# Optimization experiments

Hardware: AMD Instinct MI355X
Metric: run time of the kernel (lower is better)

The kernel has to match this reference:

```python
import jax, jax.numpy as jnp
import numpy as np
import math

EPS = 1e-5

def sinusoidal_pe(seq_len, d_model, dtype=jnp.float32):
    pos = jnp.arange(seq_len, dtype=jnp.float32)[:, None]
    div = jnp.exp(jnp.arange(0, d_model, 2, dtype=jnp.float32) * (-math.log(10000.0) / d_model))
    pe = jnp.zeros((seq_len, d_model), dtype=jnp.float32)
    pe = pe.at[:, 0::2].set(jnp.sin(pos * div))
    pe = pe.at[:, 1::2].set(jnp.cos(pos * div))
    return pe.astype(dtype)

def rel_shift(pos_score):
    # pos_score: [B, H, S, S] -> Transformer-XL relative shift
    B, H, S1, S2 = pos_score.shape
    padded = jnp.pad(pos_score, ((0, 0), (0, 0), (0, 0), (1, 0)))  # [B,H,S1,S2+1]
    return padded.reshape(B, H, S2 + 1, S1)[:, :, 1:, :].reshape(B, H, S1, S2)

def setup_inputs() -> dict:
    key = jax.random.key(0)
    B, S, D, H = 4, 2048, 512, 8
    dh = D // H
    ks = jax.random.split(key, 12)
    scale = 0.02
    inp = {
        'inputs': jax.random.normal(ks[0], (B, S, D), dtype=jnp.float32),
        'gamma': jnp.ones((D,), jnp.float32),
        'beta': jnp.zeros((D,), jnp.float32),
        'Wq': jax.random.normal(ks[1], (D, D), jnp.float32) * scale,
        'bq': jnp.zeros((D,), jnp.float32),
        'Wk': jax.random.normal(ks[2], (D, D), jnp.float32) * scale,
        'bk': jnp.zeros((D,), jnp.float32),
        'Wv': jax.random.normal(ks[3], (D, D), jnp.float32) * scale,
        'bv': jnp.zeros((D,), jnp.float32),
        'Wpos': jax.random.normal(ks[4], (D, D), jnp.float32) * scale,
        'u_bias': jax.random.normal(ks[5], (H, dh), jnp.float32) * scale,
        'v_bias': jax.random.normal(ks[6], (H, dh), jnp.float32) * scale,
        'Wo': jax.random.normal(ks[7], (D, D), jnp.float32) * scale,
        'bo': jnp.zeros((D,), jnp.float32),
    }
    return inp

def reference(inputs, gamma, beta, Wq, bq, Wk, bk, Wv, bv, Wpos, u_bias, v_bias, Wo, bo):
    B, S, D = inputs.shape
    H, dh = u_bias.shape
    # relative positional encoding (same for each batch element)
    pos_emb = sinusoidal_pe(S, D)  # [S, D]
    # pre-norm
    mu = jnp.mean(inputs, axis=-1, keepdims=True)
    var = jnp.var(inputs, axis=-1, keepdims=True)
    x = (inputs - mu) * jax.lax.rsqrt(var + EPS) * gamma + beta
    # projections (torch Linear: y = x @ W.T + b)
    q = (x @ Wq.T + bq).reshape(B, S, H, dh)
    k = (x @ Wk.T + bk).reshape(B, S, H, dh)
    v = (x @ Wv.T + bv).reshape(B, S, H, dh)
    pos = (pos_emb @ Wpos.T).reshape(S, H, dh)
    # content and position scores
    content = jnp.einsum('bshd,bthd->bhst', q + u_bias, k)
    pos_score = jnp.einsum('bshd,thd->bhst', q + v_bias, pos)
    pos_score = rel_shift(pos_score)
    score = (content + pos_score) / jnp.sqrt(jnp.float32(D))
    attn = jax.nn.softmax(score, axis=-1)  # dropout = identity (eval mode)
    ctx = jnp.einsum('bhst,bthd->bshd', attn, v).reshape(B, S, D)
    out = ctx @ Wo.T + bo
    return out  # module dropout = identity in eval
```

## Files before the change

### kernel.cpp

```cpp
#include <hip/hip_runtime.h>
#include <math.h>

typedef unsigned short u16;
typedef unsigned int u32;
typedef __bf16 bf16x8 __attribute__((ext_vector_type(8)));
typedef float f32x4 __attribute__((ext_vector_type(4)));

#define SEQ 2048
#define DM  512
#define NH  8
#define DH  64
#define SP  2064
#define PE_ROWS 2304
#define MFMA(a,b,c) __builtin_amdgcn_mfma_f32_16x16x32_bf16(a,b,c,0,0,0)

__device__ __forceinline__ u16 f2bf(float f) {
  union { float f; u32 u; } x; x.f = f;
  u32 u = x.u;
  u32 r = u + 0x7fffu + ((u >> 16) & 1u);
  return (u16)(r >> 16);
}
__device__ __forceinline__ float bf2f(u16 h) {
  union { u32 u; float f; } x; x.u = ((u32)h) << 16;
  return x.f;
}
__device__ __forceinline__ f32x4 fzero() { f32x4 z = {0.f,0.f,0.f,0.f}; return z; }

__device__ __forceinline__ void gl16(const u16* g, u16* l) {
  __builtin_amdgcn_global_load_lds((const __attribute__((address_space(1))) void*)g,
                                   (__attribute__((address_space(3))) void*)l, 16, 0, 0);
}

__global__ __launch_bounds__(256) void k_ingest(const void* g_, const void* be_, const void* wq_, const void* bq_,
                                                const void* wk_, const void* bk_, const void* wv_, const void* bv_,
                                                const void* wp_, const void* ub_, const void* vb_, const void* wo_,
                                                const void* bo_, u16* __restrict__ dst) {
  int idx8 = blockIdx.x * 256 + threadIdx.x;
  int base = idx8 * 8;
  const void* p; int loc;
  if (base < 786432)       { int w = base >> 18; p = (w==0)?wq_:((w==1)?wk_:wv_); loc = base & 262143; }
  else if (base < 1048576) { p = wp_; loc = base - 786432; }
  else if (base < 1310720) { p = wo_; loc = base - 1048576; }
  else if (base < 1312256) { int o = base - 1310720; int w = o >> 9; p = (w==0)?bq_:((w==1)?bk_:bv_); loc = o & 511; }
  else if (base < 1312768) { p = bo_; loc = base - 1312256; }
  else if (base < 1313280) { p = g_;  loc = base - 1312768; }
  else if (base < 1313792) { p = be_; loc = base - 1313280; }
  else if (base < 1314304) { p = ub_; loc = base - 1313792; }
  else                     { p = vb_; loc = base - 1314304; }
  bool f32 = (((const u16*)g_)[0] == 0);
  union { uint4 q; u16 s[8]; } o;
  if (f32) {
    const float* s = (const float*)p + loc;
    float4 f0 = *(const float4*)s, f1 = *(const float4*)(s + 4);
    o.s[0]=f2bf(f0.x); o.s[1]=f2bf(f0.y); o.s[2]=f2bf(f0.z); o.s[3]=f2bf(f0.w);
    o.s[4]=f2bf(f1.x); o.s[5]=f2bf(f1.y); o.s[6]=f2bf(f1.z); o.s[7]=f2bf(f1.w);
  } else {
    o.q = *(const uint4*)((const u16*)p + loc);
  }
  *(uint4*)(dst + base) = o.q;
}

__global__ __launch_bounds__(256) void k_init(u16* pe, u16* pos_ext, u16* qupad, u16* qvpad) {
  int idx = blockIdx.x * 256 + threadIdx.x;
  {
    int s = idx >> 8, c = idx & 255;
    float div = __expf((float)(2*c) * (-0.017988946039015986f));
    float ang = (float)s * div;
    pe[s * DM + 2*c]     = f2bf(__sinf(ang));
    pe[s * DM + 2*c + 1] = f2bf(__cosf(ang));
  }
  if (idx < 131072) {
    int h = idx >> 14;
    int r2 = (idx >> 6) & 255;
    int d = idx & 63;
    int row = (r2 < 128) ? r2 : (2048 + r2);
    pos_ext[((size_t)h * PE_ROWS + row) * DH + d] = 0;
  }
  if (idx < 32768) {
    int bh = idx >> 10;
    int r = (idx >> 6) & 15;
    int d = idx & 63;
    size_t off = ((size_t)bh * SP + 2048 + r) * DH + d;
    qupad[off] = 0; qvpad[off] = 0;
  }
}

__global__ __launch_bounds__(256) void k_ln(const void* __restrict__ inraw,
                                            const u16* __restrict__ gamma,
                                            const u16* __restrict__ beta,
                                            const u16* __restrict__ probe,
                                            u16* __restrict__ xout) {
  int wave = threadIdx.x >> 6, lane = threadIdx.x & 63;
  int row = blockIdx.x * 4 + wave;
  bool f32in = (probe[0] == 0);
  float v[8], sum = 0.f, sq = 0.f;
  if (f32in) {
    const float* s = (const float*)inraw + (size_t)row * DM + lane * 8;
    float4 f0 = *(const float4*)s, f1 = *(const float4*)(s + 4);
    v[0]=f0.x; v[1]=f0.y; v[2]=f0.z; v[3]=f0.w; v[4]=f1.x; v[5]=f1.y; v[6]=f1.z; v[7]=f1.w;
  } else {
    union { uint4 q; u16 s[8]; } raw;
    raw.q = *(const uint4*)((const u16*)inraw + (size_t)row * DM + lane * 8);
    for (int j = 0; j < 8; j++) v[j] = bf2f(raw.s[j]);
  }
  for (int j = 0; j < 8; j++) { sum += v[j]; sq += v[j]*v[j]; }
  for (int off = 1; off < 64; off <<= 1) { sum += __shfl_xor(sum, off); sq += __shfl_xor(sq, off); }
  float mu = sum * (1.0f/512.0f);
  float var = sq * (1.0f/512.0f) - mu*mu;
  float rs = 1.0f / sqrtf(var + 1e-5f);
  union { uint4 q; u16 s[8]; } gr, br, ov;
  gr.q = *(const uint4*)(gamma + lane*8);
  br.q = *(const uint4*)(beta + lane*8);
  for (int j = 0; j < 8; j++) ov.s[j] = f2bf((v[j]-mu)*rs*bf2f(gr.s[j]) + bf2f(br.s[j]));
  *(uint4*)(xout + (size_t)row*DM + lane*8) = ov.q;
}

__global__ __launch_bounds__(256) void k_gemm2(const u16* __restrict__ A,
                                               const u16* __restrict__ W,
                                               const u16* __restrict__ bias,
                                               const u16* __restrict__ ub,
                                               const u16* __restrict__ vb,
                                               u16* __restrict__ o_qu,
                                               u16* __restrict__ o_qv,
                                               u16* __restrict__ o_k,
                                               u16* __restrict__ o_v,
                                               void* __restrict__ og,
                                               const u16* __restrict__ probe,
                                               int mode, int gy) {
  __shared__ __align__(16) u16 As[128*32];
  __shared__ __align__(16) u16 Bs[64*32];
  int nwg = gridDim.x;
  int bid = blockIdx.x;
  int swz = (bid & 7) * (nwg >> 3) + (bid >> 3);
  int m0 = (swz / gy) * 128, n0 = (swz % gy) * 64;
  int tid = threadIdx.x;
  int wave = tid >> 6, lane = tid & 63, lg = lane >> 4, lr = lane & 15;
  int wm = (wave >> 1) * 64, wn = (wave & 1) * 32;
  const u16* Ap = A + (size_t)(m0 + (tid >> 2)) * 512 + (tid & 3) * 8;
  const u16* Wp = W + (size_t)(n0 + (tid >> 2)) * 512 + (tid & 3) * 8;
  u16* AsB = As + wave * 512;
  u16* BsB = Bs + wave * 512;
  f32x4 acc[4][2];
  for (int i=0;i<4;i++) for (int j=0;j<2;j++) acc[i][j] = fzero();
  for (int k0 = 0; k0 < 512; k0 += 32) {
    __syncthreads();
    gl16(Ap + k0, AsB);
    gl16(Ap + k0 + 64*512, AsB + 2048);
    gl16(Wp + k0, BsB);
    __syncthreads();
    bf16x8 af[4], bfr[2];
    for (int mt=0; mt<4; mt++) af[mt] = *(const bf16x8*)&As[(wm + mt*16 + lr)*32 + lg*8];
    for (int nt=0; nt<2; nt++) bfr[nt] = *(const bf16x8*)&Bs[(wn + nt*16 + lr)*32 + lg*8];
    __builtin_amdgcn_s_setprio(1);
    for (int mt=0; mt<4; mt++)
      for (int nt=0; nt<2; nt++)
        acc[mt][nt] = MFMA(af[mt], bfr[nt], acc[mt][nt]);
    __builtin_amdgcn_s_setprio(0);
  }
  const float iscale = 0.044194173824159216f;
  for (int mt=0; mt<4; mt++) for (int nt=0; nt<2; nt++) {
    int gcol = n0 + wn + nt*16 + lr;
    float bv = bias ? bf2f(bias[gcol]) : 0.0f;
    for (int r=0; r<4; r++) {
      int grow = m0 + wm + mt*16 + lg*4 + r;
      float val = acc[mt][nt][r] + bv;
      if (mode == 4) {
        int sect = gcol >> 9;
        int col = gcol & 511;
        int h = col >> 6, d = col & 63;
        int bb = grow >> 11, s = grow & 2047;
        if (sect == 0) {
          size_t o = ((size_t)(bb*8 + h) * SP + s) * 64 + d;
          o_qu[o] = f2bf((val + bf2f(ub[col])) * iscale);
          o_qv[o] = f2bf((val + bf2f(vb[col])) * iscale);
        } else if (sect == 1) {
          o_k[((size_t)(bb*8 + h) * 2048 + s) * 64 + d] = f2bf(val);
        } else {
          o_v[((size_t)(bb*8 + h) * 2048 + s) * 64 + d] = f2bf(val);
        }
      } else if (mode == 0) {
        size_t o = (size_t)grow * 512 + gcol;
        if (probe[0] == 0) ((float*)og)[o] = val;
        else               ((u16*)og)[o] = f2bf(val);
      } else {
        int h = gcol >> 6, d = gcol & 63;
        ((u16*)og)[((size_t)h * PE_ROWS + 128 + grow) * 64 + d] = f2bf(val);
      }
    }
  }
}

__global__ __launch_bounds__(256) void k_attn(const u16* __restrict__ qu,
                                              const u16* __restrict__ qv,
                                              const u16* __restrict__ kk,
                                              const u16* __restrict__ vv,
                                              const u16* __restrict__ posx,
                                              u16* __restrict__ ctx) {
  __shared__ __align__(16) u16 Ks[64*64];
  __shared__ __align__(16) u16 Vt[64*64];
  __shared__ __align__(16) u16 Pw[128*64];
  __shared__ __align__(16) u16 UtPp[4*1536];

  int d0b = blockIdx.x;
  int ii = d0b >> 3;
  int bh = (d0b & 7) * 4 + (ii >> 5);
  int qb = ii & 31;
  int h = bh & 7, b = bh >> 3;
  int i0 = qb * 64;
  int tid = threadIdx.x;
  int wave = tid >> 6, lane = tid & 63, lg = lane >> 4, lr = lane & 15;
  int wm16 = wave * 16;
  int bw = 48 - wm16;

  const u16* quB = qu + ((size_t)bh * SP + i0 + wm16 + lr) * 64;
  const u16* qvB = qv + ((size_t)bh * SP + i0 + wm16 + lr) * 64;
  const u16* qvS = qv + ((size_t)bh * SP + i0 + wm16 + 1 + lr) * 64;
  bf16x8 a_qu[2], a_qv[2], a_qs[2];
  for (int k2 = 0; k2 < 2; k2++) {
    a_qu[k2] = *(const bf16x8*)(quB + k2*32 + lg*8);
    a_qv[k2] = *(const bf16x8*)(qvB + k2*32 + lg*8);
    a_qs[k2] = *(const bf16x8*)(qvS + k2*32 + lg*8);
  }

  f32x4 oacc[4];
  for (int dt=0; dt<4; dt++) oacc[dt] = fzero();
  float mrun[4], lrun[4];
  for (int r=0;r<4;r++){ mrun[r] = -INFINITY; lrun[r] = 0.0f; }

  u16* Utw = UtPp + wave * 1536;
  const u16* Kg0 = kk + (size_t)bh * 2048 * 64;
  const u16* Vg0 = vv + (size_t)bh * 2048 * 64;
  const u16* Pgh = posx + (size_t)h * PE_ROWS * 64;
  int vc8 = tid & 7, vn2 = tid >> 3;

  for (int j0 = 0; j0 < 2048; j0 += 64) {
    bool low = (j0 <= i0);
    int pb1 = 2112 - i0 + j0;
    int pb2 = 63 + j0 - i0;
    __syncthreads();
    {
      const u16* Kg = Kg0 + (size_t)j0 * 64;
      #pragma unroll
      for (int p = 0; p < 2; p++) {
        int t = p*256 + tid;
        int row = t >> 3;
        int c8s = (t & 7) ^ (row & 7);
        gl16(Kg + row*64 + c8s*8, Ks + p*2048 + wave*512);
      }
    }
    {
      const u16* Pg = Pgh + (size_t)(low ? pb1 : pb2) * 64;
      #pragma unroll
      for (int p = 0; p < 4; p++) {
        int t = p*256 + tid;
        int row = t >> 3;
        int c8s = (t & 7) ^ (row & 7);
        gl16(Pg + row*64 + c8s*8, Pw + p*2048 + wave*512);
      }
    }
    {
      const u16* Vg = Vg0 + (size_t)j0 * 64 + (size_t)(vn2*2) * 64 + vc8*8;
      union { uint4 q; u16 s[8]; } t0, t1;
      t0.q = *(const uint4*)(Vg);
      t1.q = *(const uint4*)(Vg + 64);
      int n = vn2 * 2;
      #pragma unroll
      for (int e = 0; e < 8; e++) {
        int d = vc8*8 + e;
        u32 pk2 = (u32)t0.s[e] | ((u32)t1.s[e] << 16);
        int colp = n ^ ((((d & 7) ^ (d >> 3)) & 7) << 3);
        *(u32*)&Vt[d*64 + colp] = pk2;
      }
    }
    __syncthreads();

    f32x4 c4[4];
    __builtin_amdgcn_s_setprio(1);
    for (int nt = 0; nt < 4; nt++) {
      int rw = nt*16 + lr;
      bf16x8 b0 = *(const bf16x8*)&Ks[rw*64 + ((lg ^ (rw&7)) << 3)];
      bf16x8 b1 = *(const bf16x8*)&Ks[rw*64 + (((4+lg) ^ (rw&7)) << 3)];
      f32x4 z = fzero();
      z = MFMA(a_qu[0], b0, z);
      z = MFMA(a_qu[1], b1, z);
      c4[nt] = z;
    }
    __builtin_amdgcn_s_setprio(0);

    auto uphase = [&](bf16x8 A0, bf16x8 A1, int pm) {
      __builtin_amdgcn_s_setprio(1);
      #pragma unroll
      for (int wt = 0; wt < 5; wt++) {
        int rw = bw + wt*16 + lr;
        bf16x8 b0 = *(const bf16x8*)&Pw[rw*64 + ((lg ^ (rw&7)) << 3)];
        bf16x8 b1 = *(const bf16x8*)&Pw[rw*64 + (((4+lg) ^ (rw&7)) << 3)];
        f32x4 z = fzero();
        z = MFMA(A0, b0, z);
        z = MFMA(A1, b1, z);
        u32 r0, r1;
        asm("v_cvt_pk_bf16_f32 %0, %1, %2" : "=v"(r0) : "v"(z[0]), "v"(z[1]));
        asm("v_cvt_pk_bf16_f32 %0, %1, %2" : "=v"(r1) : "v"(z[2]), "v"(z[3]));
        int wloc = wt*16 + lr;
        int a = wloc*16 + ((lg ^ ((wloc >> 2) & 3)) << 2);
        uint2 pr; pr.x = r0; pr.y = r1;
        *(uint2*)&Utw[a] = pr;
      }
      __builtin_amdgcn_s_setprio(0);
      asm volatile("s_waitcnt lgkmcnt(0)" ::: "memory");
      #pragma unroll
      for (int nt = 0; nt < 4; nt++) {
        int n = nt*16 + lr;
        #pragma unroll
        for (int r = 0; r < 4; r++) {
          int rowl = lg*4 + r;
          int wl = n - rowl + 15;
          float uval = bf2f(Utw[wl*16 + (((rowl>>2) ^ ((wl>>2)&3)) << 2) + (rowl&3)]);
          if (pm == 0) c4[nt][r] += uval;
          else {
            int delta = (j0 + n) - (i0 + wm16 + rowl);
            bool use = (pm == 1) ? (delta <= 0) : (delta >= 2);
            if (use) c4[nt][r] += uval;
          }
        }
      }
    };

    if (j0 < i0) uphase(a_qv[0], a_qv[1], 0);
    else if (j0 == i0) {
      uphase(a_qv[0], a_qv[1], 1);
      __syncthreads();
      {
        const u16* Pg = Pgh + (size_t)pb2 * 64;
        #pragma unroll
        for (int p = 0; p < 4; p++) {
          int t = p*256 + tid;
          int row = t >> 3;
          int c8s = (t & 7) ^ (row & 7);
          gl16(Pg + row*64 + c8s*8, Pw + p*2048 + wave*512);
        }
      }
      __syncthreads();
      uphase(a_qs[0], a_qs[1], 2);
    } else if (j0 == i0 + 64) {
      uphase(a_qs[0], a_qs[1], 2);
    } else {
      uphase(a_qs[0], a_qs[1], 0);
    }

    float sfac[4];
    for (int r=0;r<4;r++) {
      float mx = fmaxf(fmaxf(c4[0][r], c4[1][r]), fmaxf(c4[2][r], c4[3][r]));
      for (int off=1; off<16; off<<=1) mx = fmaxf(mx, __shfl_xor(mx, off));
      float mn = fmaxf(mrun[r], mx);
      sfac[r] = __expf(mrun[r] - mn);
      mrun[r] = mn;
    }
    u16* Ppw = Utw;
    float rs[4] = {0.f, 0.f, 0.f, 0.f};
    #pragma unroll
    for (int nt=0;nt<4;nt++) {
      int n = nt*16 + lr;
      #pragma unroll
      for (int rp = 0; rp < 2; rp++) {
        int ri = rp*2;
        float p0 = __expf(c4[nt][ri]   - mrun[ri]);
        float p1 = __expf(c4[nt][ri+1] - mrun[ri+1]);
        rs[ri] += p0; rs[ri+1] += p1;
        u32 pk;
        asm("v_cvt_pk_bf16_f32 %0, %1, %2" : "=v"(pk) : "v"(p0), "v"(p1));
        int rowl0 = lg*4 + ri;
        Ppw[rowl0*64 + (n ^ ((rowl0&7)<<3))] = (u16)pk;
        int rowl1 = rowl0 + 1;
        Ppw[rowl1*64 + (n ^ ((rowl1&7)<<3))] = (u16)(pk >> 16);
      }
    }
    for (int r=0;r<4;r++) {
      for (int off=1; off<16; off<<=1) rs[r] += __shfl_xor(rs[r], off);
      lrun[r] = lrun[r]*sfac[r] + rs[r];
    }
    for (int dt=0;dt<4;dt++)
      for (int r=0;r<4;r++) oacc[dt][r] *= sfac[r];

    asm volatile("s_waitcnt lgkmcnt(0)" ::: "memory");
    bf16x8 pa0 = *(const bf16x8*)&Ppw[lr*64 + ((lg ^ (lr&7)) << 3)];
    bf16x8 pa1 = *(const bf16x8*)&Ppw[lr*64 + (((4+lg) ^ (lr&7)) << 3)];
    __builtin_amdgcn_s_setprio(1);
    for (int dt=0;dt<4;dt++) {
      int rw = dt*16 + lr;
      int sw = (rw & 7) ^ ((rw >> 3) & 7);
      bf16x8 b0 = *(const bf16x8*)&Vt[rw*64 + ((lg ^ sw) << 3)];
      bf16x8 b1 = *(const bf16x8*)&Vt[rw*64 + (((4+lg) ^ sw) << 3)];
      oacc[dt] = MFMA(pa0, b0, oacc[dt]);
      oacc[dt] = MFMA(pa1, b1, oacc[dt]);
    }
    __builtin_amdgcn_s_setprio(0);
  }

  float inv[4];
  for (int r=0;r<4;r++) inv[r] = 1.0f / lrun[r];
  for (int dt=0;dt<4;dt++) {
    for (int r=0;r<4;r++) {
      int rowg = i0 + wm16 + lg*4 + r;
      size_t o = ((size_t)b * 2048 + rowg) * 512 + h*64 + dt*16 + lr;
      ctx[o] = f2bf(oacc[dt][r] * inv[r]);
    }
  }
}

extern "C" void kernel_launch(void* const* d_in, const int* in_sizes, int n_in,
                              void* d_out, int out_size, void* d_ws, size_t ws_size,
                              hipStream_t stream) {
  (void)in_sizes; (void)n_in; (void)out_size; (void)ws_size;

  char* ws = (char*)d_ws;
  u16* params = (u16*)(ws);
  u16* pe   = (u16*)(ws + 2629632);
  u16* x    = (u16*)(ws + 4726784);
  u16* quA  = (u16*)(ws + 13115392);
  u16* qvA  = (u16*)(ws + 21569536);
  u16* kA   = (u16*)(ws + 30023680);
  u16* vA   = (u16*)(ws + 38412288);
  u16* posx = (u16*)(ws + 46800896);
  u16* ctx  = (u16*)(ws + 49160192);

  const u16* Wqkv   = params + 0;
  const u16* Wpos   = params + 786432;
  const u16* Wo     = params + 1048576;
  const u16* bqkv   = params + 1310720;
  const u16* bo     = params + 1312256;
  const u16* gamma  = params + 1312768;
  const u16* beta   = params + 1313280;
  const u16* ub     = params + 1313792;
  const u16* vb     = params + 1314304;
  const u16* probe  = (const u16*)d_in[1];

  k_ingest<<<dim3(642), dim3(256), 0, stream>>>(d_in[1], d_in[2], d_in[3], d_in[4], d_in[5],
                                                d_in[6], d_in[7], d_in[8], d_in[9], d_in[10],
                                                d_in[11], d_in[12], d_in[13], params);
  k_init<<<dim3(2048), dim3(256), 0, stream>>>(pe, posx, quA, qvA);
  k_ln<<<dim3(2048), dim3(256), 0, stream>>>(d_in[0], gamma, beta, probe, x);
  k_gemm2<<<dim3(1536), dim3(256), 0, stream>>>(x, Wqkv, bqkv, ub, vb, quA, qvA, kA, vA,
                                                nullptr, probe, 4, 24);
  k_gemm2<<<dim3(128), dim3(256), 0, stream>>>(pe, Wpos, nullptr, nullptr, nullptr,
                                               nullptr, nullptr, nullptr, nullptr,
                                               (void*)posx, probe, 3, 8);
  k_attn<<<dim3(1024), dim3(256), 0, stream>>>(quA, qvA, kA, vA, posx, ctx);
  k_gemm2<<<dim3(512), dim3(256), 0, stream>>>(ctx, Wo, bo, nullptr, nullptr,
                                               nullptr, nullptr, nullptr, nullptr,
                                               d_out, probe, 0, 8);
}
```

Measured before the change: 348.0 us.

## Prefetch next K/pos/V tile into registers while computing current tile

Replaces the direct global-to-LDS loads of the K, positional and V tiles with register-staged loads. The next tile is fetched into registers during the current iteration's compute and written to LDS at the start of the following iteration. The goal is to hide global memory latency behind the MFMA and softmax work. The cost is about 32 extra VGPRs per thread, which may lower occupancy, and the LDS writes now go through registers instead of the direct-to-LDS path.

```diff
diff --git a/kernel.cpp b/kernel.cpp
--- a/kernel.cpp
+++ b/kernel.cpp
@@ -228,50 +228,68 @@
   for (int r=0;r<4;r++){ mrun[r] = -INFINITY; lrun[r] = 0.0f; }
 
   u16* Utw = UtPp + wave * 1536;
+  u16* Ppw = Utw;
   const u16* Kg0 = kk + (size_t)bh * 2048 * 64;
   const u16* Vg0 = vv + (size_t)bh * 2048 * 64;
   const u16* Pgh = posx + (size_t)h * PE_ROWS * 64;
   int vc8 = tid & 7, vn2 = tid >> 3;
 
-  for (int j0 = 0; j0 < 2048; j0 += 64) {
-    bool low = (j0 <= i0);
-    int pb1 = 2112 - i0 + j0;
-    int pb2 = 63 + j0 - i0;
+  uint4 kreg0, kreg1, preg0, preg1, preg2, preg3, vreg0, vreg1;
+  auto loadTile = [&](int j0s) {
+    const u16* Kg = Kg0 + (size_t)j0s * 64;
+    {
+      int t2 = tid;
+      int row = t2 >> 3, c8s = (t2 & 7) ^ (row & 7);
+      kreg0 = *(const uint4*)(Kg + row*64 + c8s*8);
+      t2 = 256 + tid;
+      row = t2 >> 3; c8s = (t2 & 7) ^ (row & 7);
+      kreg1 = *(const uint4*)(Kg + row*64 + c8s*8);
+    }
+    bool low = (j0s <= i0);
+    int pb = low ? (2112 - i0 + j0s) : (63 + j0s - i0);
+    const u16* Pg = Pgh + (size_t)pb * 64;
+    {
+      int t2 = tid;
+      int row = t2 >> 3, c8s = (t2 & 7) ^ (row & 7);
+      preg0 = *(const uint4*)(Pg + row*64 + c8s*8);
+      t2 = 256 + tid; row = t2 >> 3; c8s = (t2 & 7) ^ (row & 7);
+      preg1 = *(const uint4*)(Pg + row*64 + c8s*8);
+      t2 = 512 + tid; row = t2 >> 3; c8s = (t2 & 7) ^ (row & 7);
+      preg2 = *(const uint4*)(Pg + row*64 + c8s*8);
+      t2 = 768 + tid; row = t2 >> 3; c8s = (t2 & 7) ^ (row & 7);
+      preg3 = *(const uint4*)(Pg + row*64 + c8s*8);
+    }
+    const u16* Vg = Vg0 + (size_t)j0s * 64 + (size_t)(vn2*2) * 64 + vc8*8;
+    vreg0 = *(const uint4*)(Vg);
+    vreg1 = *(const uint4*)(Vg + 64);
+  };
+
+  auto writeTile = [&]() {
+    *(uint4*)&Ks[(0*256 + tid)*8] = kreg0;
+    *(uint4*)&Ks[(1*256 + tid)*8] = kreg1;
+    *(uint4*)&Pw[(0*256 + tid)*8] = preg0;
+    *(uint4*)&Pw[(1*256 + tid)*8] = preg1;
+    *(uint4*)&Pw[(2*256 + tid)*8] = preg2;
+    *(uint4*)&Pw[(3*256 + tid)*8] = preg3;
+    union { uint4 q; u16 s[8]; } t0, t1;
+    t0.q = vreg0; t1.q = vreg1;
+    int n = vn2 * 2;
+    #pragma unroll
+    for (int e = 0; e < 8; e++) {
+      int d = vc8*8 + e;
+      u32 pk2 = (u32)t0.s[e] | ((u32)t1.s[e] << 16);
+      int colp = n ^ ((((d & 7) ^ (d >> 3)) & 7) << 3);
+      *(u32*)&Vt[d*64 + colp] = pk2;
+    }
+  };
+
+  loadTile(0);
+
+  for (int t = 0; t < 32; t++) {
+    int j0 = t * 64;
     __syncthreads();
-    {
-      const u16* Kg = Kg0 + (size_t)j0 * 64;
-      #pragma unroll
-      for (int p = 0; p < 2; p++) {
-        int t = p*256 + tid;
-        int row = t >> 3;
-        int c8s = (t & 7) ^ (row & 7);
-        gl16(Kg + row*64 + c8s*8, Ks + p*2048 + wave*512);
-      }
-    }
-    {
-      const u16* Pg = Pgh + (size_t)(low ? pb1 : pb2) * 64;
-      #pragma unroll
-      for (int p = 0; p < 4; p++) {
-        int t = p*256 + tid;
-        int row = t >> 3;
-        int c8s = (t & 7) ^ (row & 7);
-        gl16(Pg + row*64 + c8s*8, Pw + p*2048 + wave*512);
-      }
-    }
-    {
-      const u16* Vg = Vg0 + (size_t)j0 * 64 + (size_t)(vn2*2) * 64 + vc8*8;
-      union { uint4 q; u16 s[8]; } t0, t1;
-      t0.q = *(const uint4*)(Vg);
-      t1.q = *(const uint4*)(Vg + 64);
-      int n = vn2 * 2;
-      #pragma unroll
-      for (int e = 0; e < 8; e++) {
-        int d = vc8*8 + e;
-        u32 pk2 = (u32)t0.s[e] | ((u32)t1.s[e] << 16);
-        int colp = n ^ ((((d & 7) ^ (d >> 3)) & 7) << 3);
-        *(u32*)&Vt[d*64 + colp] = pk2;
-      }
-    }
+    writeTile();
+    if (t < 31) loadTile(j0 + 64);
     __syncthreads();
 
     f32x4 c4[4];
@@ -330,12 +348,13 @@
       uphase(a_qv[0], a_qv[1], 1);
       __syncthreads();
       {
+        int pb2 = 63 + j0 - i0;
         const u16* Pg = Pgh + (size_t)pb2 * 64;
         #pragma unroll
         for (int p = 0; p < 4; p++) {
-          int t = p*256 + tid;
-          int row = t >> 3;
-          int c8s = (t & 7) ^ (row & 7);
+          int tt = p*256 + tid;
+          int row = tt >> 3;
+          int c8s = (tt & 7) ^ (row & 7);
           gl16(Pg + row*64 + c8s*8, Pw + p*2048 + wave*512);
         }
       }
@@ -355,7 +374,6 @@
       sfac[r] = __expf(mrun[r] - mn);
       mrun[r] = mn;
     }
-    u16* Ppw = Utw;
     float rs[4] = {0.f, 0.f, 0.f, 0.f};
     #pragma unroll
     for (int nt=0;nt<4;nt++) {
```

After: 464.7 us. 1.34x slower.
